# Kernel optimization log

Hardware: AMD Instinct MI355X
Metric: run time of the kernel (lower is better)

The kernel has to match this reference:

```python
import jax, jax.numpy as jnp
import numpy as np
import math

D = 2048          # embedding_size
H = 16            # nheads
HD = D // H       # head_dim
S = 2048          # seq_len
B = 2
# SwiGLU hidden per source: int(2*(4*D)/3) rounded up to multiple of 256
FF = 256 * ((int(2 * (4 * D) / 3) + 255) // 256)  # 5632
EPS = 1e-6


def pe_row(seq_len, d_model):
    # PositionalEncoding buffer, but forward uses only pe[:, seq_len-1]
    pos = float(seq_len - 1)
    div = jnp.exp(jnp.arange(0, d_model, 2, dtype=jnp.float32) * (-math.log(10000.0) / d_model))
    row = jnp.zeros((d_model,), jnp.float32)
    row = row.at[0::2].set(jnp.sin(pos * div))
    row = row.at[1::2].set(jnp.cos(pos * div))
    return row  # [D]


def rmsnorm(x, g, eps=EPS):
    xf = x.astype(jnp.float32)
    n = xf * jax.lax.rsqrt(jnp.mean(xf * xf, axis=-1, keepdims=True) + eps)
    return g * n.astype(x.dtype)


def setup_inputs() -> dict:
    key = jax.random.key(0)
    ks = jax.random.split(key, 16)
    sd = 0.02
    x = jax.random.normal(ks[0], (B, S, D), jnp.float32)
    mask = jnp.triu(jnp.ones((S, S), jnp.int32), k=1)[None, None]  # [1,1,S,S], 1 = masked
    return {
        'x': x,
        'mask': mask,
        'qkv_w': jax.random.normal(ks[1], (3 * D, D), jnp.float32) * sd,
        'qkv_b': jnp.zeros((3 * D,), jnp.float32),
        'fc_w': jax.random.normal(ks[2], (D, D), jnp.float32) * sd,
        'fc_b': jnp.zeros((D,), jnp.float32),
        'w1': jax.random.normal(ks[3], (FF, D), jnp.float32) * sd,
        'b1': jnp.zeros((FF,), jnp.float32),
        'w2': jax.random.normal(ks[4], (FF, D), jnp.float32) * sd,
        'b2': jnp.zeros((FF,), jnp.float32),
        'w3': jax.random.normal(ks[5], (D, FF), jnp.float32) * sd,
        'b3': jnp.zeros((D,), jnp.float32),
        'g_attn': jnp.ones((D,), jnp.float32),
        'g_ff': jnp.ones((D,), jnp.float32),
    }


def _block(x, mask, qkv_w, qkv_b, fc_w, fc_b, w1, b1, w2, b2, w3, b3, g_attn, g_ff):
    b, s, _ = x.shape
    # attention sublayer (pre-norm)
    h_in = rmsnorm(x, g_attn)
    qkv = h_in @ qkv_w.T + qkv_b
    xq, xk, xv = jnp.split(qkv, 3, axis=-1)
    pe = pe_row(s, D)  # single row added everywhere (faithful to source)
    xq = xq + pe
    xk = xk + pe
    q = xq.reshape(b, s, H, HD).transpose(0, 2, 1, 3)
    k = xk.reshape(b, s, H, HD).transpose(0, 2, 1, 3)
    v = xv.reshape(b, s, H, HD).transpose(0, 2, 1, 3)
    scores = jnp.einsum('bhqd,bhkd->bhqk', q, k) / math.sqrt(HD)
    scores = jnp.where(mask == 1, jnp.float32(-1e9), scores)
    attn = jax.nn.softmax(scores, axis=-1)
    out = jnp.einsum('bhqk,bhkd->bhqd', attn, v)
    out = out.transpose(0, 2, 1, 3).reshape(b, s, D)
    attn_out = out @ fc_w.T + fc_b
    h = x + attn_out
    # SwiGLU FFN sublayer (pre-norm)
    f_in = rmsnorm(h, g_ff)
    gate = jax.nn.silu(f_in @ w1.T + b1) * (f_in @ w2.T + b2)
    return h + gate @ w3.T + b3


def reference(x, mask, qkv_w, qkv_b, fc_w, fc_b, w1, b1, w2, b2, w3, b3, g_attn, g_ff):
    return _block(x, mask, qkv_w, qkv_b, fc_w, fc_b, w1, b1, w2, b2, w3, b3, g_attn, g_ff)
```

## Files before the change

### kernel.cpp

```cpp
#include <hip/hip_runtime.h>
#include <math.h>


typedef __attribute__((ext_vector_type(8))) short bf16x8;
typedef __attribute__((ext_vector_type(4))) short bf16x4;
typedef __attribute__((ext_vector_type(4))) float f32x4;

#define DEVI __device__ __forceinline__

DEVI unsigned short f2bf(float f) {
  unsigned u = __builtin_bit_cast(unsigned, f);
  u += 0x7FFFu + ((u >> 16) & 1u);
  return (unsigned short)(u >> 16);
}
DEVI float bf2f(unsigned short h) {
  unsigned u = ((unsigned)h) << 16;
  return __builtin_bit_cast(float, u);
}

#define GLL16(g, l) __builtin_amdgcn_global_load_lds( \
    (const __attribute__((address_space(1))) unsigned int*)(const void*)(g), \
    (__attribute__((address_space(3))) unsigned int*)(void*)(l), 16, 0, 0)

__global__ __launch_bounds__(256) void wconv_k(const float* __restrict__ src,
                                               unsigned short* __restrict__ dst,
                                               long n8) {
  long t = (long)blockIdx.x * 256 + threadIdx.x;
  if (t >= n8) return;
  const f32x4* s = (const f32x4*)(src + t * 8);
  f32x4 a = s[0], b = s[1];
  bf16x8 o;
#pragma unroll
  for (int j = 0; j < 4; ++j) {
    o[j]     = (short)f2bf(a[j]);
    o[4 + j] = (short)f2bf(b[j]);
  }
  *(bf16x8*)(dst + t * 8) = o;
}

__global__ void pe_k(float* __restrict__ pe) {
  int c = blockIdx.x * 256 + threadIdx.x;
  if (c >= 2048) return;
  int i2 = c & ~1;
  float div = __expf(-(float)i2 * (9.210340371976184f / 2048.0f));
  float ang = 2047.0f * div;
  pe[c] = (c & 1) ? cosf(ang) : sinf(ang);
}

__global__ __launch_bounds__(256) void rmsnorm_k(const float* __restrict__ x,
                                                 const float* __restrict__ g,
                                                 unsigned short* __restrict__ out) {
  long row = blockIdx.x;
  const float* xr = x + row * 2048;
  int tid = threadIdx.x;
  f32x4 v0 = *(const f32x4*)&xr[tid * 8];
  f32x4 v1 = *(const f32x4*)&xr[tid * 8 + 4];
  float ss = 0.f;
#pragma unroll
  for (int j = 0; j < 4; ++j) ss += v0[j] * v0[j] + v1[j] * v1[j];
#pragma unroll
  for (int m = 1; m < 64; m <<= 1) ss += __shfl_xor(ss, m, 64);
  __shared__ float red[4];
  int lane = tid & 63, wv = tid >> 6;
  if (lane == 0) red[wv] = ss;
  __syncthreads();
  float tot = red[0] + red[1] + red[2] + red[3];
  float rn = rsqrtf(tot * (1.0f / 2048.0f) + 1e-6f);
  const float* gr = g + tid * 8;
  bf16x8 o;
#pragma unroll
  for (int j = 0; j < 4; ++j) {
    o[j]     = (short)f2bf(v0[j] * rn * gr[j]);
    o[4 + j] = (short)f2bf(v1[j] * rn * gr[4 + j]);
  }
  *(bf16x8*)&out[row * 2048 + tid * 8] = o;
}

template <int EPI>
__global__ __launch_bounds__(256) void gemm_bt(const unsigned short* __restrict__ A,
                                               const unsigned short* __restrict__ W,
                                               const float* __restrict__ bias,
                                               const float* __restrict__ resid,
                                               void* __restrict__ outv,
                                               int M, int N, int K) {
  __shared__ __align__(16) unsigned short lds[2][2][128 * 32];
  const int tid  = threadIdx.x;
  const int lane = tid & 63;
  const int wv   = tid >> 6;
  const int wr   = wv >> 1;
  const int wc   = wv & 1;
  const int l15  = lane & 15;
  const int lk   = (lane >> 4) << 3;
  const long tm  = (long)blockIdx.y * 128;
  const long tn  = (long)blockIdx.x * 128;

  const int srw = tid >> 2;
  const int scc = (tid & 3) << 3;
  const unsigned short* gA = A + (tm + srw) * (long)K + scc;
  const unsigned short* gB = W + (tn + srw) * (long)K + scc;
  const long rowstep = 64L * K;

  f32x4 acc[4][4] = {};

#define STAGE(buf, k0) do {                                   \
    unsigned short* lA = &lds[buf][0][(wv * 16) * 32];        \
    unsigned short* lB = &lds[buf][1][(wv * 16) * 32];        \
    GLL16(gA + (k0), lA);                                     \
    GLL16(gA + (k0) + rowstep, lA + 64 * 32);                 \
    GLL16(gB + (k0), lB);                                     \
    GLL16(gB + (k0) + rowstep, lB + 64 * 32);                 \
  } while (0)

  const int KT = K >> 5;
  STAGE(0, 0);
  int cur = 0;
  for (int kt = 0; kt < KT; ++kt) {
    __syncthreads();
    if (kt + 1 < KT) STAGE(cur ^ 1, (long)(kt + 1) << 5);
    const unsigned short* lA = &lds[cur][0][0];
    const unsigned short* lB = &lds[cur][1][0];
    bf16x8 af[4], bfv[4];
#pragma unroll
    for (int m = 0; m < 4; ++m)
      af[m] = *(const bf16x8*)&lA[(wr * 64 + m * 16 + l15) * 32 + lk];
#pragma unroll
    for (int n = 0; n < 4; ++n)
      bfv[n] = *(const bf16x8*)&lB[(wc * 64 + n * 16 + l15) * 32 + lk];
#pragma unroll
    for (int m = 0; m < 4; ++m)
#pragma unroll
      for (int n = 0; n < 4; ++n)
        acc[m][n] = __builtin_amdgcn_mfma_f32_16x16x32_bf16(af[m], bfv[n], acc[m][n], 0, 0, 0);
    cur ^= 1;
  }
#undef STAGE

  const long row0 = tm + wr * 64 + ((lane >> 4) << 2);
  const long col0 = tn + wc * 64;
#pragma unroll
  for (int n = 0; n < 4; ++n) {
    const long col = col0 + n * 16 + l15;
    const float bv = bias[col];
#pragma unroll
    for (int m = 0; m < 4; ++m) {
      const long rw = row0 + m * 16;
#pragma unroll
      for (int j = 0; j < 4; ++j) {
        const float v = acc[m][n][j] + bv;
        if (EPI == 0) {
          ((unsigned short*)outv)[(rw + j) * (long)N + col] = f2bf(v);
        } else {
          float* of = (float*)outv;
          const long i = (rw + j) * (long)N + col;
          of[i] = resid[i] + v;
        }
      }
    }
  }
}

__global__ __launch_bounds__(256) void krepack_k(const unsigned short* __restrict__ qkv,
                                                 const float* __restrict__ pe,
                                                 unsigned short* __restrict__ kpe) {
  long t = (long)blockIdx.x * 256 + threadIdx.x;
  long idx = t * 8;
  long row = idx >> 11;
  int cd  = (int)(idx & 2047);
  int h = cd >> 7, d = cd & 127;
  long b = row >> 11, s = row & 2047;
  bf16x8 v = *(const bf16x8*)&qkv[row * 6144 + 2048 + cd];
  const float* per = &pe[cd];
#pragma unroll
  for (int j = 0; j < 8; ++j)
    v[j] = (short)f2bf(bf2f((unsigned short)v[j]) + per[j]);
  *(bf16x8*)&kpe[(((b * 16 + h)) * 2048 + s) * 128 + d] = v;
}

__global__ __launch_bounds__(256) void vtrans_k(const unsigned short* __restrict__ qkv,
                                                unsigned short* __restrict__ Vt) {
  const int s0 = blockIdx.x * 64;
  const int d0 = blockIdx.y * 64;
  const int bh = blockIdx.z;
  const long b = bh >> 4;
  const int h = bh & 15;
  __shared__ unsigned short tile[64][76];
  const int t = threadIdx.x;
#pragma unroll
  for (int half = 0; half < 2; ++half) {
    int c = t + half * 256;
    int r = c >> 3;
    int cc = (c & 7) * 8;
    bf16x8 v = *(const bf16x8*)&qkv[(b * 2048 + s0 + r) * 6144 + 4096 + h * 128 + d0 + cc];
#pragma unroll
    for (int j = 0; j < 8; ++j) tile[cc + j][r] = (unsigned short)v[j];
  }
  __syncthreads();
#pragma unroll
  for (int half = 0; half < 2; ++half) {
    int c = t + half * 256;
    int dr = c >> 3;
    int sc = (c & 7) * 8;
    bf16x4 lo = *(const bf16x4*)&tile[dr][sc];
    bf16x4 hi = *(const bf16x4*)&tile[dr][sc + 4];
    bf16x8 v;
#pragma unroll
    for (int j = 0; j < 4; ++j) { v[j] = lo[j]; v[4 + j] = hi[j]; }
    *(bf16x8*)&Vt[((long)bh * 128 + d0 + dr) * 2048 + s0 + sc] = v;
  }
}

__global__ __launch_bounds__(256, 2) void fattn_k(const unsigned short* __restrict__ QKV,
                                                  const float* __restrict__ pe,
                                                  const unsigned short* __restrict__ Kp,
                                                  const unsigned short* __restrict__ Vt,
                                                  unsigned short* __restrict__ O) {
  const int lin = blockIdx.x;
  const int chunk = lin & 7;
  const int idx = lin >> 3;
  const int bh = chunk * 4 + (idx >> 4);
  const int i16 = idx & 15;
  const int qb = (i16 & 1) ? ((i16 - 1) >> 1) : (15 - (i16 >> 1));
  const long b = bh >> 4;
  const int h = bh & 15;
  const int q0 = qb * 128;
  const int tid = threadIdx.x, lane = tid & 63, wv = tid >> 6;
  const int l15 = lane & 15, lg = lane >> 4;
  const int qw = q0 + wv * 32;

  __shared__ __align__(16) unsigned short Kl[2][8192];
  __shared__ __align__(16) unsigned short Vl[2][8192];
  __shared__ __align__(16) unsigned short Plds[4][32][40];

  const float scale = 0.08838834764831845f;
  const unsigned short* Qb = QKV + (b * 2048 + qw) * 6144 + h * 128;
  bf16x8 qf[2][4];
#pragma unroll
  for (int r = 0; r < 2; ++r)
#pragma unroll
    for (int kc = 0; kc < 4; ++kc) {
      bf16x8 v = *(const bf16x8*)&Qb[(r * 16 + l15) * 6144 + kc * 32 + lg * 8];
      const float* per = &pe[h * 128 + kc * 32 + lg * 8];
#pragma unroll
      for (int j = 0; j < 8; ++j)
        v[j] = (short)f2bf((bf2f((unsigned short)v[j]) + per[j]) * scale);
      qf[r][kc] = v;
    }

  const unsigned short* Kg = Kp + (long)bh * 2048 * 128;
  const unsigned short* Vg = Vt + (long)bh * 128 * 2048;

  auto stage = [&](int buf, int key0) {
#pragma unroll
    for (int ld = 0; ld < 4; ++ld) {
      int sr = wv * 16 + ld * 4 + (lane >> 4);
      int sc = ((lane & 15) << 3) ^ ((sr & 7) << 3);
      GLL16(Kg + (long)(key0 + sr) * 128 + sc, &Kl[buf][wv * 2048 + ld * 512]);
      int dr = wv * 32 + ld * 8 + (lane >> 3);
      int dc = ((lane & 7) << 3) ^ ((dr & 7) << 3);
      GLL16(Vg + (long)dr * 2048 + key0 + dc, &Vl[buf][wv * 2048 + ld * 512]);
    }
  };

  f32x4 o[2][8] = {};
  float mr[2][4], sdn[2][4];
#pragma unroll
  for (int r = 0; r < 2; ++r)
#pragma unroll
    for (int j = 0; j < 4; ++j) { mr[r][j] = -1e30f; sdn[r][j] = 0.f; }

  const int nkt = (q0 >> 6) + 2;
  stage(0, 0);
  __syncthreads();
  int cur = 0;
  for (int kt = 0; kt < nkt; ++kt) {
    const int key0 = kt << 6;
    if (kt + 1 < nkt) stage(cur ^ 1, key0 + 64);
    if (key0 <= qw + 31) {
      f32x4 s[2][4] = {};
      __builtin_amdgcn_s_setprio(1);
#pragma unroll
      for (int ks = 0; ks < 4; ++ks) {
        bf16x8 kf[4];
#pragma unroll
        for (int kc = 0; kc < 4; ++kc)
          kf[kc] = *(const bf16x8*)&Kl[cur][(ks * 16 + l15) * 128 +
                                           ((kc * 32 + lg * 8) ^ ((l15 & 7) << 3))];
#pragma unroll
        for (int r = 0; r < 2; ++r)
#pragma unroll
          for (int kc = 0; kc < 4; ++kc)
            s[r][ks] = __builtin_amdgcn_mfma_f32_16x16x32_bf16(qf[r][kc], kf[kc], s[r][ks], 0, 0, 0);
      }
      __builtin_amdgcn_s_setprio(0);
      const bool maskt = (key0 + 63 > qw);
      float pm[2][4];
#pragma unroll
      for (int r = 0; r < 2; ++r)
#pragma unroll
        for (int j = 0; j < 4; ++j) pm[r][j] = -1e30f;
#pragma unroll
      for (int r = 0; r < 2; ++r)
#pragma unroll
        for (int ks = 0; ks < 4; ++ks)
#pragma unroll
          for (int j = 0; j < 4; ++j) {
            float v = s[r][ks][j];
            if (maskt) {
              int qrow = qw + r * 16 + lg * 4 + j;
              int key  = key0 + ks * 16 + l15;
              v = (key <= qrow) ? v : -1e30f;
              s[r][ks][j] = v;
            }
            pm[r][j] = fmaxf(pm[r][j], v);
          }
#pragma unroll
      for (int msk = 1; msk < 16; msk <<= 1)
#pragma unroll
        for (int r = 0; r < 2; ++r)
#pragma unroll
          for (int j = 0; j < 4; ++j) pm[r][j] = fmaxf(pm[r][j], __shfl_xor(pm[r][j], msk, 64));
      bool grow = false;
#pragma unroll
      for (int r = 0; r < 2; ++r)
#pragma unroll
        for (int j = 0; j < 4; ++j) grow = grow || (pm[r][j] > mr[r][j] + 8.0f);
      if (__any(grow)) {
#pragma unroll
        for (int r = 0; r < 2; ++r)
#pragma unroll
          for (int j = 0; j < 4; ++j) {
            float mn = fmaxf(mr[r][j], pm[r][j]);
            float corr = __expf(mr[r][j] - mn);
            mr[r][j] = mn;
            sdn[r][j] *= corr;
#pragma unroll
            for (int nf = 0; nf < 8; ++nf) o[r][nf][j] *= corr;
          }
      }
      float ps[2][4];
#pragma unroll
      for (int r = 0; r < 2; ++r)
#pragma unroll
        for (int j = 0; j < 4; ++j) ps[r][j] = 0.f;
#pragma unroll
      for (int r = 0; r < 2; ++r)
#pragma unroll
        for (int ks = 0; ks < 4; ++ks)
#pragma unroll
          for (int j = 0; j < 4; ++j) {
            float e = __expf(s[r][ks][j] - mr[r][j]);
            s[r][ks][j] = e;
            ps[r][j] += e;
          }
#pragma unroll
      for (int msk = 1; msk < 16; msk <<= 1)
#pragma unroll
        for (int r = 0; r < 2; ++r)
#pragma unroll
          for (int j = 0; j < 4; ++j) ps[r][j] += __shfl_xor(ps[r][j], msk, 64);
#pragma unroll
      for (int r = 0; r < 2; ++r)
#pragma unroll
        for (int j = 0; j < 4; ++j) sdn[r][j] += ps[r][j];
#pragma unroll
      for (int hk = 0; hk < 2; ++hk) {
#pragma unroll
        for (int r = 0; r < 2; ++r)
#pragma unroll
          for (int ks2 = 0; ks2 < 2; ++ks2)
#pragma unroll
            for (int j = 0; j < 4; ++j)
              Plds[wv][r * 16 + lg * 4 + j][ks2 * 16 + l15] = f2bf(s[r][hk * 2 + ks2][j]);
        bf16x8 pf[2];
#pragma unroll
        for (int r = 0; r < 2; ++r) {
          bf16x4 lo = *(const bf16x4*)&Plds[wv][r * 16 + l15][lg * 8];
          bf16x4 hi = *(const bf16x4*)&Plds[wv][r * 16 + l15][lg * 8 + 4];
          bf16x8 p;
#pragma unroll
          for (int j = 0; j < 4; ++j) { p[j] = lo[j]; p[4 + j] = hi[j]; }
          pf[r] = p;
        }
        __builtin_amdgcn_s_setprio(1);
#pragma unroll
        for (int nf = 0; nf < 8; ++nf) {
          bf16x8 vf = *(const bf16x8*)&Vl[cur][(nf * 16 + l15) * 64 +
                                              ((hk * 32 + lg * 8) ^ ((l15 & 7) << 3))];
#pragma unroll
          for (int r = 0; r < 2; ++r)
            o[r][nf] = __builtin_amdgcn_mfma_f32_16x16x32_bf16(pf[r], vf, o[r][nf], 0, 0, 0);
        }
        __builtin_amdgcn_s_setprio(0);
      }
    }
    __syncthreads();
    cur ^= 1;
  }
  unsigned short* Ob = O + (b * 2048 + qw) * 2048 + h * 128;
#pragma unroll
  for (int r = 0; r < 2; ++r)
#pragma unroll
    for (int j = 0; j < 4; ++j) {
      float inv = 1.0f / sdn[r][j];
#pragma unroll
      for (int nf = 0; nf < 8; ++nf)
        Ob[(long)(r * 16 + lg * 4 + j) * 2048 + nf * 16 + l15] = f2bf(o[r][nf][j] * inv);
    }
}

__global__ __launch_bounds__(256) void gate_k(const unsigned short* __restrict__ a1,
                                              const unsigned short* __restrict__ a2,
                                              unsigned short* __restrict__ g) {
  long idx = ((long)blockIdx.x * 256 + threadIdx.x) * 8;
  bf16x8 x1 = *(const bf16x8*)&a1[idx];
  bf16x8 x2 = *(const bf16x8*)&a2[idx];
  bf16x8 r;
#pragma unroll
  for (int j = 0; j < 8; ++j) {
    float f1 = bf2f((unsigned short)x1[j]);
    float f2v = bf2f((unsigned short)x2[j]);
    float sg = f1 / (1.0f + __expf(-f1));
    r[j] = (short)f2bf(sg * f2v);
  }
  *(bf16x8*)&g[idx] = r;
}

extern "C" void kernel_launch(void* const* d_in, const int* in_sizes, int n_in,
                              void* d_out, int out_size, void* d_ws, size_t ws_size,
                              hipStream_t stream) {
  (void)in_sizes; (void)n_in; (void)out_size; (void)ws_size;
  const float* x    = (const float*)d_in[0];
  const float* qkvw = (const float*)d_in[2];
  const float* qkvb = (const float*)d_in[3];
  const float* fcw  = (const float*)d_in[4];
  const float* fcb  = (const float*)d_in[5];
  const float* w1   = (const float*)d_in[6];
  const float* b1   = (const float*)d_in[7];
  const float* w2   = (const float*)d_in[8];
  const float* b2   = (const float*)d_in[9];
  const float* w3   = (const float*)d_in[10];
  const float* b3   = (const float*)d_in[11];
  const float* ga   = (const float*)d_in[12];
  const float* gf   = (const float*)d_in[13];

  char* ws = (char*)d_ws;
  size_t off = 0;
  auto alloc = [&](size_t bytes) -> char* {
    char* p = ws + off;
    off = (off + bytes + 255) & ~(size_t)255;
    return p;
  };
  unsigned short* wqkv  = (unsigned short*)alloc(6144L * 2048 * 2);
  unsigned short* wfc   = (unsigned short*)alloc(2048L * 2048 * 2);
  unsigned short* w1b   = (unsigned short*)alloc(5632L * 2048 * 2);
  unsigned short* w2b   = (unsigned short*)alloc(5632L * 2048 * 2);
  unsigned short* w3b   = (unsigned short*)alloc(2048L * 5632 * 2);
  float*          pe    = (float*)alloc(2048 * 4);
  unsigned short* hin   = (unsigned short*)alloc(4096L * 2048 * 2);
  unsigned short* qkv   = (unsigned short*)alloc(4096L * 6144 * 2);
  unsigned short* kpe   = (unsigned short*)alloc(4096L * 2048 * 2);
  unsigned short* Vt    = (unsigned short*)alloc(4096L * 2048 * 2);
  unsigned short* attnb = (unsigned short*)alloc(4096L * 2048 * 2);
  float* h = (float*)d_out;

  wconv_k<<<6144, 256, 0, stream>>>(qkvw, wqkv, 6144L * 2048 / 8);
  wconv_k<<<2048, 256, 0, stream>>>(fcw,  wfc,  2048L * 2048 / 8);
  wconv_k<<<5632, 256, 0, stream>>>(w1,   w1b,  5632L * 2048 / 8);
  wconv_k<<<5632, 256, 0, stream>>>(w2,   w2b,  5632L * 2048 / 8);
  wconv_k<<<5632, 256, 0, stream>>>(w3,   w3b,  2048L * 5632 / 8);
  pe_k<<<8, 256, 0, stream>>>(pe);

  rmsnorm_k<<<4096, 256, 0, stream>>>(x, ga, hin);
  gemm_bt<0><<<dim3(48, 32), 256, 0, stream>>>(hin, wqkv, qkvb, nullptr, qkv, 4096, 6144, 2048);
  krepack_k<<<4096, 256, 0, stream>>>(qkv, pe, kpe);
  vtrans_k<<<dim3(32, 2, 32), 256, 0, stream>>>(qkv, Vt);
  fattn_k<<<dim3(512), 256, 0, stream>>>(qkv, pe, kpe, Vt, attnb);
  gemm_bt<1><<<dim3(16, 32), 256, 0, stream>>>(attnb, wfc, fcb, x, h, 4096, 2048, 2048);

  rmsnorm_k<<<4096, 256, 0, stream>>>(h, gf, hin);
  unsigned short* a1 = qkv;
  unsigned short* a2 = kpe;
  gemm_bt<0><<<dim3(44, 32), 256, 0, stream>>>(hin, w1b, b1, nullptr, a1, 4096, 5632, 2048);
  gemm_bt<0><<<dim3(44, 32), 256, 0, stream>>>(hin, w2b, b2, nullptr, a2, 4096, 5632, 2048);
  gate_k<<<11264, 256, 0, stream>>>(a1, a2, a1);
  gemm_bt<1><<<dim3(16, 32), 256, 0, stream>>>(a1, w3b, b3, h, d_out, 4096, 2048, 5632);
}
```

Baseline: 780.8 us.

## Replace GEMM with 256x128 tile, triple-buffered LDS pipeline and XCD-aware block mapping

Replaces the 128x128, double-buffered, K=32 GEMM with a 512-thread kernel that computes 256x128 tiles. It steps K by 64, keeps three LDS stages with an XOR swizzle to avoid bank conflicts, and uses fine-grained waitcnt/barrier scheduling plus s_setprio around the MFMA bursts. Blocks are remapped round-robin across 8 XCDs to improve L2 locality. The aim is more arithmetic intensity and better overlap of global loads with MFMA, at the cost of more LDS per block and occupancy limited to one block per CU.

```diff
diff --git a/kernel.cpp b/kernel.cpp
--- a/kernel.cpp
+++ b/kernel.cpp
@@ -77,66 +77,92 @@
 }
 
 template <int EPI>
-__global__ __launch_bounds__(256) void gemm_bt(const unsigned short* __restrict__ A,
-                                               const unsigned short* __restrict__ W,
-                                               const float* __restrict__ bias,
-                                               const float* __restrict__ resid,
-                                               void* __restrict__ outv,
-                                               int M, int N, int K) {
-  __shared__ __align__(16) unsigned short lds[2][2][128 * 32];
+__global__ __launch_bounds__(512, 1) void gemm256(const unsigned short* __restrict__ A,
+                                                  const unsigned short* __restrict__ W,
+                                                  const float* __restrict__ bias,
+                                                  const float* __restrict__ resid,
+                                                  void* __restrict__ outv,
+                                                  int M, int N, int K, int nbx) {
+  __shared__ __align__(16) unsigned short Ab[3][256 * 64];
+  __shared__ __align__(16) unsigned short Bb[3][128 * 64];
   const int tid  = threadIdx.x;
   const int lane = tid & 63;
   const int wv   = tid >> 6;
-  const int wr   = wv >> 1;
-  const int wc   = wv & 1;
+  const int wm   = wv >> 1;
+  const int wn   = wv & 1;
   const int l15  = lane & 15;
-  const int lk   = (lane >> 4) << 3;
-  const long tm  = (long)blockIdx.y * 128;
-  const long tn  = (long)blockIdx.x * 128;
-
-  const int srw = tid >> 2;
-  const int scc = (tid & 3) << 3;
-  const unsigned short* gA = A + (tm + srw) * (long)K + scc;
-  const unsigned short* gB = W + (tn + srw) * (long)K + scc;
-  const long rowstep = 64L * K;
+  const int lg   = lane >> 4;
+  const int cpx = gridDim.x >> 3;
+  const int wg  = (blockIdx.x & 7) * cpx + (blockIdx.x >> 3);
+  const long tm = (long)(wg / nbx) * 256;
+  const long tn = (long)(wg % nbx) * 128;
+
+  const int srow = wv * 8 + (lane >> 3);
+  const int scol = (((lane & 7) ^ (lane >> 3)) << 3);
+  const unsigned short* gA = A + (tm + srow) * (long)K + scol;
+  const unsigned short* gB = W + (tn + srow) * (long)K + scol;
+
+  const int KT = K >> 6;
+
+#define STGA(buf, kt, g) GLL16(gA + ((long)(g) * 64) * K + ((long)(kt) << 6), \
+                               &Ab[buf][(g) * 4096 + wv * 512])
+#define STGB(buf, kt, g) GLL16(gB + ((long)(g) * 64) * K + ((long)(kt) << 6), \
+                               &Bb[buf][(g) * 4096 + wv * 512])
 
   f32x4 acc[4][4] = {};
 
-#define STAGE(buf, k0) do {                                   \
-    unsigned short* lA = &lds[buf][0][(wv * 16) * 32];        \
-    unsigned short* lB = &lds[buf][1][(wv * 16) * 32];        \
-    GLL16(gA + (k0), lA);                                     \
-    GLL16(gA + (k0) + rowstep, lA + 64 * 32);                 \
-    GLL16(gB + (k0), lB);                                     \
-    GLL16(gB + (k0) + rowstep, lB + 64 * 32);                 \
-  } while (0)
-
-  const int KT = K >> 5;
-  STAGE(0, 0);
-  int cur = 0;
-  for (int kt = 0; kt < KT; ++kt) {
-    __syncthreads();
-    if (kt + 1 < KT) STAGE(cur ^ 1, (long)(kt + 1) << 5);
-    const unsigned short* lA = &lds[cur][0][0];
-    const unsigned short* lB = &lds[cur][1][0];
-    bf16x8 af[4], bfv[4];
-#pragma unroll
-    for (int m = 0; m < 4; ++m)
-      af[m] = *(const bf16x8*)&lA[(wr * 64 + m * 16 + l15) * 32 + lk];
-#pragma unroll
-    for (int n = 0; n < 4; ++n)
-      bfv[n] = *(const bf16x8*)&lB[(wc * 64 + n * 16 + l15) * 32 + lk];
-#pragma unroll
-    for (int m = 0; m < 4; ++m)
+  STGA(0, 0, 0); STGA(0, 0, 1); STGA(0, 0, 2); STGA(0, 0, 3);
+  STGB(0, 0, 0); STGB(0, 0, 1);
+  STGA(1, 1, 0); STGA(1, 1, 1); STGA(1, 1, 2); STGA(1, 1, 3);
+  STGB(1, 1, 0); STGB(1, 1, 1);
+  asm volatile("s_waitcnt vmcnt(6)" ::: "memory");
+  __builtin_amdgcn_s_barrier();
+
+  int ct = 0;
+  for (int t = 0; t < KT; ++t) {
+    const int pt = (ct >= 1) ? (ct - 1) : 2;
+    const bool pre = (t + 2) < KT;
+    const unsigned short* At = &Ab[ct][0];
+    const unsigned short* Bt = &Bb[ct][0];
+#pragma unroll
+    for (int kk = 0; kk < 2; ++kk) {
+      bf16x8 af[4], bfv[4];
+#pragma unroll
+      for (int m = 0; m < 4; ++m)
+        af[m] = *(const bf16x8*)&At[((wm * 64 + m * 16 + l15) * 8 +
+                                     ((kk * 4 + lg) ^ (l15 & 7))) * 8];
 #pragma unroll
       for (int n = 0; n < 4; ++n)
-        acc[m][n] = __builtin_amdgcn_mfma_f32_16x16x32_bf16(af[m], bfv[n], acc[m][n], 0, 0, 0);
-    cur ^= 1;
-  }
-#undef STAGE
-
-  const long row0 = tm + wr * 64 + ((lane >> 4) << 2);
-  const long col0 = tn + wc * 64;
+        bfv[n] = *(const bf16x8*)&Bt[((wn * 64 + n * 16 + l15) * 8 +
+                                      ((kk * 4 + lg) ^ (l15 & 7))) * 8];
+      if (pre) {
+        if (kk == 0) { STGA(pt, t + 2, 0); STGA(pt, t + 2, 1); STGA(pt, t + 2, 2); }
+        else         { STGA(pt, t + 2, 3); STGB(pt, t + 2, 0); STGB(pt, t + 2, 1); }
+      }
+      __builtin_amdgcn_s_barrier();
+      __builtin_amdgcn_s_setprio(1);
+#pragma unroll
+      for (int m = 0; m < 4; ++m)
+#pragma unroll
+        for (int n = 0; n < 4; ++n)
+          acc[m][n] = __builtin_amdgcn_mfma_f32_16x16x32_bf16(af[m], bfv[n], acc[m][n], 0, 0, 0);
+      __builtin_amdgcn_s_setprio(0);
+      if (kk == 0) {
+        __builtin_amdgcn_s_barrier();
+      } else {
+        if (t + 2 < KT)      asm volatile("s_waitcnt vmcnt(6)" ::: "memory");
+        else if (t + 1 < KT) asm volatile("s_waitcnt vmcnt(0)" ::: "memory");
+        __builtin_amdgcn_s_barrier();
+      }
+    }
+    ct = (ct + 1 >= 3) ? 0 : (ct + 1);
+  }
+#undef STGA
+#undef STGB
+  __builtin_amdgcn_sched_barrier(0);
+
+  const long row0 = tm + wm * 64 + (lg << 2);
+  const long col0 = tn + wn * 64;
 #pragma unroll
   for (int n = 0; n < 4; ++n) {
     const long col = col0 + n * 16 + l15;
@@ -471,17 +497,17 @@
   pe_k<<<8, 256, 0, stream>>>(pe);
 
   rmsnorm_k<<<4096, 256, 0, stream>>>(x, ga, hin);
-  gemm_bt<0><<<dim3(48, 32), 256, 0, stream>>>(hin, wqkv, qkvb, nullptr, qkv, 4096, 6144, 2048);
+  gemm256<0><<<768, 512, 0, stream>>>(hin, wqkv, qkvb, nullptr, qkv, 4096, 6144, 2048, 48);
   krepack_k<<<4096, 256, 0, stream>>>(qkv, pe, kpe);
   vtrans_k<<<dim3(32, 2, 32), 256, 0, stream>>>(qkv, Vt);
   fattn_k<<<dim3(512), 256, 0, stream>>>(qkv, pe, kpe, Vt, attnb);
-  gemm_bt<1><<<dim3(16, 32), 256, 0, stream>>>(attnb, wfc, fcb, x, h, 4096, 2048, 2048);
+  gemm256<1><<<256, 512, 0, stream>>>(attnb, wfc, fcb, x, h, 4096, 2048, 2048, 16);
 
   rmsnorm_k<<<4096, 256, 0, stream>>>(h, gf, hin);
   unsigned short* a1 = qkv;
   unsigned short* a2 = kpe;
-  gemm_bt<0><<<dim3(44, 32), 256, 0, stream>>>(hin, w1b, b1, nullptr, a1, 4096, 5632, 2048);
-  gemm_bt<0><<<dim3(44, 32), 256, 0, stream>>>(hin, w2b, b2, nullptr, a2, 4096, 5632, 2048);
+  gemm256<0><<<704, 512, 0, stream>>>(hin, w1b, b1, nullptr, a1, 4096, 5632, 2048, 44);
+  gemm256<0><<<704, 512, 0, stream>>>(hin, w2b, b2, nullptr, a2, 4096, 5632, 2048, 44);
   gate_k<<<11264, 256, 0, stream>>>(a1, a2, a1);
-  gemm_bt<1><<<dim3(16, 32), 256, 0, stream>>>(a1, w3b, b3, h, d_out, 4096, 2048, 5632);
-}
+  gemm256<1><<<256, 512, 0, stream>>>(a1, w3b, b3, h, d_out, 4096, 2048, 5632, 16);
+}
```

Result: no change. 772.8 us (-1.0%).

## Fuse SwiGLU gate into second FFN GEMM epilogue and split attention launch

Applied to the files above, without the earlier changes.

The w2 GEMM gains a third epilogue mode that reads the w1 activations, applies SiLU, and writes the gated product in place. This removes the separate gate kernel and one bf16 intermediate round-trip of 4096x5632 elements. The flash-attention launch is also split into two 256-block launches, first the upper query-block half and then the lower half, with a qbase parameter. The split changes scheduling and load balance across the causal work, and adds one extra kernel launch.

```diff
diff --git a/kernel.cpp b/kernel.cpp
--- a/kernel.cpp
+++ b/kernel.cpp
@@ -80,7 +80,7 @@
 __global__ __launch_bounds__(256) void gemm_bt(const unsigned short* __restrict__ A,
                                                const unsigned short* __restrict__ W,
                                                const float* __restrict__ bias,
-                                               const float* __restrict__ resid,
+                                               const void* __restrict__ residv,
                                                void* __restrict__ outv,
                                                int M, int N, int K) {
   __shared__ __align__(16) unsigned short lds[2][2][128 * 32];
@@ -147,12 +147,15 @@
 #pragma unroll
       for (int j = 0; j < 4; ++j) {
         const float v = acc[m][n][j] + bv;
+        const long i = (rw + j) * (long)N + col;
         if (EPI == 0) {
-          ((unsigned short*)outv)[(rw + j) * (long)N + col] = f2bf(v);
+          ((unsigned short*)outv)[i] = f2bf(v);
+        } else if (EPI == 1) {
+          ((float*)outv)[i] = ((const float*)residv)[i] + v;
         } else {
-          float* of = (float*)outv;
-          const long i = (rw + j) * (long)N + col;
-          of[i] = resid[i] + v;
+          float f1 = bf2f(((const unsigned short*)residv)[i]);
+          float sg = f1 / (1.0f + __expf(-f1));
+          ((unsigned short*)outv)[i] = f2bf(sg * v);
         }
       }
     }
@@ -213,13 +216,14 @@
                                                   const float* __restrict__ pe,
                                                   const unsigned short* __restrict__ Kp,
                                                   const unsigned short* __restrict__ Vt,
-                                                  unsigned short* __restrict__ O) {
+                                                  unsigned short* __restrict__ O,
+                                                  int qbase) {
   const int lin = blockIdx.x;
   const int chunk = lin & 7;
   const int idx = lin >> 3;
-  const int bh = chunk * 4 + (idx >> 4);
-  const int i16 = idx & 15;
-  const int qb = (i16 & 1) ? ((i16 - 1) >> 1) : (15 - (i16 >> 1));
+  const int bh = chunk * 4 + (idx >> 3);
+  const int qsub = idx & 7;
+  const int qb = qbase + ((qsub & 1) ? (qsub >> 1) : (7 - (qsub >> 1)));
   const long b = bh >> 4;
   const int h = bh & 15;
   const int q0 = qb * 128;
@@ -406,23 +410,6 @@
       for (int nf = 0; nf < 8; ++nf)
         Ob[(long)(r * 16 + lg * 4 + j) * 2048 + nf * 16 + l15] = f2bf(o[r][nf][j] * inv);
     }
-}
-
-__global__ __launch_bounds__(256) void gate_k(const unsigned short* __restrict__ a1,
-                                              const unsigned short* __restrict__ a2,
-                                              unsigned short* __restrict__ g) {
-  long idx = ((long)blockIdx.x * 256 + threadIdx.x) * 8;
-  bf16x8 x1 = *(const bf16x8*)&a1[idx];
-  bf16x8 x2 = *(const bf16x8*)&a2[idx];
-  bf16x8 r;
-#pragma unroll
-  for (int j = 0; j < 8; ++j) {
-    float f1 = bf2f((unsigned short)x1[j]);
-    float f2v = bf2f((unsigned short)x2[j]);
-    float sg = f1 / (1.0f + __expf(-f1));
-    r[j] = (short)f2bf(sg * f2v);
-  }
-  *(bf16x8*)&g[idx] = r;
 }
 
 extern "C" void kernel_launch(void* const* d_in, const int* in_sizes, int n_in,
@@ -474,14 +461,13 @@
   gemm_bt<0><<<dim3(48, 32), 256, 0, stream>>>(hin, wqkv, qkvb, nullptr, qkv, 4096, 6144, 2048);
   krepack_k<<<4096, 256, 0, stream>>>(qkv, pe, kpe);
   vtrans_k<<<dim3(32, 2, 32), 256, 0, stream>>>(qkv, Vt);
-  fattn_k<<<dim3(512), 256, 0, stream>>>(qkv, pe, kpe, Vt, attnb);
+  fattn_k<<<dim3(256), 256, 0, stream>>>(qkv, pe, kpe, Vt, attnb, 8);
+  fattn_k<<<dim3(256), 256, 0, stream>>>(qkv, pe, kpe, Vt, attnb, 0);
   gemm_bt<1><<<dim3(16, 32), 256, 0, stream>>>(attnb, wfc, fcb, x, h, 4096, 2048, 2048);
 
   rmsnorm_k<<<4096, 256, 0, stream>>>(h, gf, hin);
   unsigned short* a1 = qkv;
-  unsigned short* a2 = kpe;
   gemm_bt<0><<<dim3(44, 32), 256, 0, stream>>>(hin, w1b, b1, nullptr, a1, 4096, 5632, 2048);
-  gemm_bt<0><<<dim3(44, 32), 256, 0, stream>>>(hin, w2b, b2, nullptr, a2, 4096, 5632, 2048);
-  gate_k<<<11264, 256, 0, stream>>>(a1, a2, a1);
+  gemm_bt<2><<<dim3(44, 32), 256, 0, stream>>>(hin, w2b, b2, a1, a1, 4096, 5632, 2048);
   gemm_bt<1><<<dim3(16, 32), 256, 0, stream>>>(a1, w3b, b3, h, d_out, 4096, 2048, 5632);
 }
```

New measurement: 792.2 us. Within noise of the previous version (+1.5%).
